# Optimization experiments

Measured on AMD Instinct MI355X. Metric: run time of the kernel, lower is better.

## Reference

```python
import jax, jax.numpy as jnp
import numpy as np

N_QUBITS = 20
W_MUL = (2.0 ** 0.5) * (5.0 ** -0.5)  # he_std = gain * 5**-0.5, use_wscale=True, lrmul=1

_C = jnp.complex64
X = jnp.array([[0, 1], [1, 0]], dtype=_C)
Y = jnp.array([[0, -1j], [1j, 0]], dtype=_C)
Z = jnp.array([[1, 0], [0, -1]], dtype=_C)
I2 = jnp.eye(2, dtype=_C)
I4 = jnp.eye(4, dtype=_C)
XX = jnp.kron(X, X)
YY = jnp.kron(Y, Y)
ZZ = jnp.kron(Z, Z)


def _rot(theta, pauli, ident):
    # exp(-i * theta/2 * P) = cos(theta/2) I - i sin(theta/2) P
    a = theta * 0.5
    return jnp.cos(a) * ident - (1j * jnp.sin(a)) * pauli


def _apply_1q(state, g, w):
    # state: [batch] + [2]*n ; contract gate input index with qubit axis w
    s = jnp.tensordot(g, state, axes=((1,), (w + 1,)))
    return jnp.moveaxis(s, 0, w + 1)


def _apply_2q(state, g4, w0, w1):
    g = g4.reshape(2, 2, 2, 2)  # (out0, out1, in0, in1)
    s = jnp.tensordot(g, state, axes=((2, 3), (w0 + 1, w1 + 1)))
    return jnp.moveaxis(s, (0, 1), (w0 + 1, w1 + 1))


def _xyz_layer(psi, params, n):
    # params: [3n]; rx, ry, rz on each wire
    for q in range(n):
        psi = _apply_1q(psi, _rot(params[3 * q], X, I2), q)
        psi = _apply_1q(psi, _rot(params[3 * q + 1], Y, I2), q)
        psi = _apply_1q(psi, _rot(params[3 * q + 2], Z, I2), q)
    return psi


def _circuit(psi, w, n):
    psi = _xyz_layer(psi, w[: 3 * n], n)
    for q in range(n - 1):
        i = 3 * n + 3 * q
        psi = _apply_2q(psi, _rot(w[i], XX, I4), q, q + 1)
        psi = _apply_2q(psi, _rot(w[i + 1], YY, I4), q, q + 1)
        psi = _apply_2q(psi, _rot(w[i + 2], ZZ, I4), q, q + 1)
    psi = _xyz_layer(psi, w[6 * n - 3 :], n)
    return psi


def setup_inputs() -> dict:
    key = jax.random.key(0)
    k1, k2 = jax.random.split(key)
    n = N_QUBITS
    dim = 1 << n
    batch = 4
    x = jax.random.normal(k1, (batch, 1, dim), dtype=jnp.float32)
    weight = jax.random.uniform(k2, (9 * n - 3,), dtype=jnp.float32, minval=0.0, maxval=2.0 * np.pi)
    return {"x": x, "weight": weight, "dimA": 10}


def reference(x, weight, dimA):
    n = N_QUBITS
    batch = x.shape[0]
    w = weight * W_MUL
    psi = x.astype(_C).reshape((batch,) + (2,) * n)  # MPS tensor [b, 2, ..., 2]
    psi = _circuit(psi, w, n)
    dimB = n - dimA
    # partial trace of |psi><psi| over the first dimB qubits (most-significant axes):
    # reduced[a, c] = sum_t psi[t, a] * conj(psi[t, c])  -- never materialize the full DM
    psi = psi.reshape(batch, 1 << dimB, 1 << dimA)
    rdm = jnp.einsum('bta,btc->bac', psi, psi.conj())
    # return real/imag stacked on last axis (real-valued representation of complex DM)
    return jnp.stack([rdm.real, rdm.imag], axis=-1)
```

## Files before the change

kernel.cpp:

```cpp
#include <hip/hip_runtime.h>
#include <hip/hip_bf16.h>

#define N_Q    20
#define DIM    (1 << N_Q)
#define BATCH  4
#define NGATES 19
#define L2OFF  117

typedef float2 c32;
typedef __attribute__((ext_vector_type(8))) short short8;
typedef __attribute__((ext_vector_type(4))) float f32x4;
typedef __attribute__((ext_vector_type(4))) unsigned int u32x4;

__device__ __forceinline__ c32 cmul(c32 a, c32 b) {
    return make_float2(fmaf(a.x, b.x, -a.y * b.y), fmaf(a.x, b.y, a.y * b.x));
}
__device__ __forceinline__ c32 cmadd(c32 acc, c32 a, c32 b) {
    acc.x = fmaf(a.x, b.x, fmaf(-a.y, b.y, acc.x));
    acc.y = fmaf(a.x, b.y, fmaf(a.y, b.x, acc.y));
    return acc;
}
__device__ __forceinline__ unsigned short f2bf(float f) {
    union { float f; unsigned u; } v; v.f = f;
    unsigned r = v.u + 0x7FFFu + ((v.u >> 16) & 1u);
    return (unsigned short)(r >> 16);
}
__device__ __forceinline__ void gll16(const void* g, void* l) {
    __builtin_amdgcn_global_load_lds((const __attribute__((address_space(1))) void*)g,
                                     (__attribute__((address_space(3))) void*)l, 16, 0, 0);
}

__device__ void mm2(const c32 A[2][2], const c32 B[2][2], c32 C[2][2]) {
    for (int i = 0; i < 2; i++)
        for (int j = 0; j < 2; j++) {
            c32 s = make_float2(0.f, 0.f);
            for (int k = 0; k < 2; k++) s = cmadd(s, A[i][k], B[k][j]);
            C[i][j] = s;
        }
}
__device__ void mm4(const c32 A[4][4], const c32 B[4][4], c32 C[4][4]) {
    for (int i = 0; i < 4; i++)
        for (int j = 0; j < 4; j++) {
            c32 s = make_float2(0.f, 0.f);
            for (int k = 0; k < 4; k++) s = cmadd(s, A[i][k], B[k][j]);
            C[i][j] = s;
        }
}
__device__ void single_u(const float* w, int base, c32 U[2][2]) {
    const float WM = 0.63245553203367586640f;
    float hx = w[base] * WM * 0.5f, hy = w[base + 1] * WM * 0.5f, hz = w[base + 2] * WM * 0.5f;
    float cx = cosf(hx), sx = sinf(hx);
    float cy = cosf(hy), sy = sinf(hy);
    float cz = cosf(hz), sz = sinf(hz);
    c32 RX[2][2] = {{{cx, 0.f}, {0.f, -sx}}, {{0.f, -sx}, {cx, 0.f}}};
    c32 RY[2][2] = {{{cy, 0.f}, {-sy, 0.f}}, {{sy, 0.f}, {cy, 0.f}}};
    c32 RZ[2][2] = {{{cz, -sz}, {0.f, 0.f}}, {{0.f, 0.f}, {cz, sz}}};
    c32 T[2][2];
    mm2(RY, RX, T);
    mm2(RZ, T, U);
}
__device__ void kron22(const c32 A[2][2], const c32 B[2][2], c32 K[4][4]) {
    for (int i = 0; i < 2; i++)
        for (int j = 0; j < 2; j++)
            for (int k = 0; k < 2; k++)
                for (int l = 0; l < 2; l++)
                    K[i * 2 + j][k * 2 + l] = cmul(A[i][k], B[j][l]);
}

__global__ void build_gates(const float* __restrict__ w, c32* __restrict__ G) {
    int q = threadIdx.x;
    if (q >= NGATES) return;
    const float WM = 0.63245553203367586640f;
    float hx = w[60 + 3 * q] * WM * 0.5f;
    float hy = w[61 + 3 * q] * WM * 0.5f;
    float hz = w[62 + 3 * q] * WM * 0.5f;
    float cx = cosf(hx), sx = sinf(hx);
    float cy = cosf(hy), sy = sinf(hy);
    float cz = cosf(hz), sz = sinf(hz);
    c32 RXX[4][4], RYY[4][4], RZZ[4][4];
    for (int i = 0; i < 4; i++)
        for (int j = 0; j < 4; j++) {
            RXX[i][j] = make_float2(0.f, 0.f);
            RYY[i][j] = make_float2(0.f, 0.f);
            RZZ[i][j] = make_float2(0.f, 0.f);
        }
    for (int i = 0; i < 4; i++) {
        RXX[i][i]     = make_float2(cx, 0.f);
        RXX[i][3 - i] = make_float2(0.f, -sx);
        RYY[i][i]     = make_float2(cy, 0.f);
    }
    RYY[0][3] = make_float2(0.f,  sy);
    RYY[1][2] = make_float2(0.f, -sy);
    RYY[2][1] = make_float2(0.f, -sy);
    RYY[3][0] = make_float2(0.f,  sy);
    RZZ[0][0] = make_float2(cz, -sz);
    RZZ[1][1] = make_float2(cz,  sz);
    RZZ[2][2] = make_float2(cz,  sz);
    RZZ[3][3] = make_float2(cz, -sz);
    c32 T[4][4], M[4][4];
    mm4(RYY, RXX, T);
    mm4(RZZ, T, M);

    c32 I2m[2][2] = {{{1.f, 0.f}, {0.f, 0.f}}, {{0.f, 0.f}, {1.f, 0.f}}};
    c32 Ua[2][2], Ub[2][2], Pre[4][4], Post[4][4];
    if (q == 0) {
        single_u(w, 0, Ua);
        single_u(w, 3, Ub);
        kron22(Ua, Ub, Pre);
    } else {
        single_u(w, 3 * (q + 1), Ub);
        kron22(I2m, Ub, Pre);
    }
    if (q == NGATES - 1) {
        single_u(w, L2OFF + 3 * 18, Ua);
        single_u(w, L2OFF + 3 * 19, Ub);
        kron22(Ua, Ub, Post);
    } else {
        single_u(w, L2OFF + 3 * q, Ua);
        kron22(Ua, I2m, Post);
    }
    c32 T2[4][4], Gq[4][4];
    mm4(M, Pre, T2);
    mm4(Post, T2, Gq);
    for (int i = 0; i < 4; i++)
        for (int j = 0; j < 4; j++)
            G[q * 16 + i * 4 + j] = Gq[i][j];
}

__device__ __forceinline__ void apply4(const c32* g, c32& x0, c32& x1, c32& x2, c32& x3) {
    c32 r0 = cmul(g[0],  x0); r0 = cmadd(r0, g[1],  x1); r0 = cmadd(r0, g[2],  x2); r0 = cmadd(r0, g[3],  x3);
    c32 r1 = cmul(g[4],  x0); r1 = cmadd(r1, g[5],  x1); r1 = cmadd(r1, g[6],  x2); r1 = cmadd(r1, g[7],  x3);
    c32 r2 = cmul(g[8],  x0); r2 = cmadd(r2, g[9],  x1); r2 = cmadd(r2, g[10], x2); r2 = cmadd(r2, g[11], x3);
    c32 r3 = cmul(g[12], x0); r3 = cmadd(r3, g[13], x1); r3 = cmadd(r3, g[14], x2); r3 = cmadd(r3, g[15], x3);
    x0 = r0; x1 = r1; x2 = r2; x3 = r3;
}
__device__ __forceinline__ void load_gate(const c32* __restrict__ gp, c32 g[16]) {
#pragma unroll
    for (int k = 0; k < 16; k++) g[k] = gp[k];
}
template <int LO>
__device__ __forceinline__ void gate_on32(c32 v[32], const c32 g[16]) {
#pragma unroll
    for (int m = 0; m < 8; ++m) {
        const int j0 = ((m >> LO) << (LO + 2)) | (m & ((1 << LO) - 1));
        const int s = 1 << LO;
        apply4(g, v[j0], v[j0 + s], v[j0 + 2 * s], v[j0 + 3 * s]);
    }
}
template <int LO>
__device__ __forceinline__ void gate_on16(c32* v, const c32 g[16]) {
#pragma unroll
    for (int m = 0; m < 4; ++m) {
        const int j0 = ((m >> LO) << (LO + 2)) | (m & ((1 << LO) - 1));
        const int s = 1 << LO;
        apply4(g, v[j0], v[j0 + s], v[j0 + 2 * s], v[j0 + 3 * s]);
    }
}

#define SIDX(l) ((l) ^ ((((l) >> 5) & 15)))

__global__ __launch_bounds__(256) void pass_a2(const float* __restrict__ x,
                                               c32* __restrict__ psi,
                                               const c32* __restrict__ Gall) {
    __shared__ __align__(16) char smem[65536];
    float* xs = (float*)smem;
    c32* s = (c32*)smem;
    int b = blockIdx.x >> 7;
    int c0 = (blockIdx.x & 127) << 5;
    const float* xp = x + ((size_t)b << 20) + c0;
    c32* pp = psi + ((size_t)b << 20) + c0;
    int t = threadIdx.x;
#pragma unroll
    for (int i = 0; i < 8; ++i) {
        int f4 = t + (i << 8);
        int row = f4 >> 3, sl = f4 & 7;
        float4 v = *reinterpret_cast<const float4*>(xp + (size_t)row * 4096 + sl * 4);
        reinterpret_cast<float4*>(xs)[row * 8 + (sl ^ (row & 7))] = v;
    }
    __syncthreads();
    int col = t & 31, rlow = t >> 5;
    c32 v[32], g[16];
#pragma unroll
    for (int j = 0; j < 32; ++j) {
        int row = (j << 3) | rlow;
        float re = xs[row * 32 + ((((col >> 2) ^ (row & 7)) << 2) | (col & 3))];
        v[j] = make_float2(re, 0.f);
    }
    __syncthreads();
    load_gate(Gall + 0 * 16, g);  gate_on32<3>(v, g);
    load_gate(Gall + 1 * 16, g);  gate_on32<2>(v, g);
    load_gate(Gall + 2 * 16, g);  gate_on32<1>(v, g);
    load_gate(Gall + 3 * 16, g);  gate_on32<0>(v, g);
#pragma unroll
    for (int j = 0; j < 32; ++j) {
        int l = ((((j << 3) | rlow) << 5)) | col;
        s[SIDX(l)] = v[j];
    }
    __syncthreads();
    int rhi = t >> 5;
#pragma unroll
    for (int rtop = 0; rtop < 2; ++rtop)
#pragma unroll
        for (int j = 0; j < 16; ++j) {
            int row = (rtop << 7) | (rhi << 4) | j;
            int l = (row << 5) | col;
            v[rtop * 16 + j] = s[SIDX(l)];
        }
    load_gate(Gall + 4 * 16, g);  gate_on16<2>(v, g);  gate_on16<2>(v + 16, g);
    load_gate(Gall + 5 * 16, g);  gate_on16<1>(v, g);  gate_on16<1>(v + 16, g);
    load_gate(Gall + 6 * 16, g);  gate_on16<0>(v, g);  gate_on16<0>(v + 16, g);
#pragma unroll
    for (int rtop = 0; rtop < 2; ++rtop)
#pragma unroll
        for (int j = 0; j < 16; ++j) {
            int row = (rtop << 7) | (rhi << 4) | j;
            pp[(size_t)row * 4096 + col] = v[rtop * 16 + j];
        }
}

__global__ __launch_bounds__(256) void pass_b2(const c32* __restrict__ psi,
                                               unsigned short* __restrict__ Brt,
                                               unsigned short* __restrict__ Bit,
                                               const c32* __restrict__ Gall) {
    __shared__ c32 s[8192];
    int b = blockIdx.x >> 7;
    int chunk = blockIdx.x & 127;
    const c32* pp = psi + ((size_t)b << 20) + ((size_t)chunk << 13);
    int t = threadIdx.x;
    c32 v[32], g[16];
#pragma unroll
    for (int j = 0; j < 32; ++j) v[j] = pp[(j << 8) | t];
    load_gate(Gall + 7 * 16, g);   gate_on32<3>(v, g);
    load_gate(Gall + 8 * 16, g);   gate_on32<2>(v, g);
    load_gate(Gall + 9 * 16, g);   gate_on32<1>(v, g);
    load_gate(Gall + 10 * 16, g);  gate_on32<0>(v, g);
#pragma unroll
    for (int j = 0; j < 32; ++j) { int l = (j << 8) | t; s[SIDX(l)] = v[j]; }
    __syncthreads();
    int hi2 = (t >> 4) << 9, lo2 = t & 15;
#pragma unroll
    for (int j = 0; j < 32; ++j) { int l = hi2 | (j << 4) | lo2; v[j] = s[SIDX(l)]; }
    load_gate(Gall + 11 * 16, g);  gate_on32<3>(v, g);
    load_gate(Gall + 12 * 16, g);  gate_on32<2>(v, g);
    load_gate(Gall + 13 * 16, g);  gate_on32<1>(v, g);
    load_gate(Gall + 14 * 16, g);  gate_on32<0>(v, g);
    __syncthreads();
#pragma unroll
    for (int j = 0; j < 32; ++j) { int l = hi2 | (j << 4) | lo2; s[SIDX(l)] = v[j]; }
    __syncthreads();
#pragma unroll
    for (int j = 0; j < 32; ++j) { int l = (t << 5) | j; v[j] = s[SIDX(l)]; }
    load_gate(Gall + 15 * 16, g);  gate_on32<3>(v, g);
    load_gate(Gall + 16 * 16, g);  gate_on32<2>(v, g);
    load_gate(Gall + 17 * 16, g);  gate_on32<1>(v, g);
    load_gate(Gall + 18 * 16, g);  gate_on32<0>(v, g);
    size_t off = ((size_t)b << 20) + ((size_t)chunk << 13) + ((size_t)t << 5);
#pragma unroll
    for (int p = 0; p < 4; ++p) {
        unsigned short rr[8], ri[8];
#pragma unroll
        for (int i = 0; i < 8; ++i) {
            rr[i] = f2bf(v[8 * p + i].x);
            ri[i] = f2bf(v[8 * p + i].y);
        }
        *reinterpret_cast<float4*>(Brt + off + 8 * p) = *reinterpret_cast<float4*>(rr);
        *reinterpret_cast<float4*>(Bit + off + 8 * p) = *reinterpret_cast<float4*>(ri);
    }
}

__global__ __launch_bounds__(256) void bt_t(const unsigned short* __restrict__ Brt,
                                            const unsigned short* __restrict__ Bit,
                                            unsigned short* __restrict__ Art,
                                            unsigned short* __restrict__ Ait) {
    __shared__ unsigned lds32[64 * 66];
    int b  = blockIdx.z;
    int t0 = blockIdx.x * 64;
    int a0 = blockIdx.y * 64;
    size_t gb = (size_t)b << 20;
#pragma unroll
    for (int h = 0; h < 2; ++h) {
        int p = threadIdx.x + h * 256;
        int r = p >> 3, cq = p & 7;
        size_t src = gb + (size_t)(t0 + r) * 1024 + a0 + cq * 8;
        float4 fr = *reinterpret_cast<const float4*>(Brt + src);
        float4 fi = *reinterpret_cast<const float4*>(Bit + src);
        const unsigned short* ur = reinterpret_cast<const unsigned short*>(&fr);
        const unsigned short* ui = reinterpret_cast<const unsigned short*>(&fi);
#pragma unroll
        for (int i = 0; i < 8; ++i)
            lds32[r * 66 + cq * 8 + i] = (unsigned)ur[i] | ((unsigned)ui[i] << 16);
    }
    __syncthreads();
#pragma unroll
    for (int h = 0; h < 2; ++h) {
        int q = threadIdx.x + h * 256;
        int a = q >> 3, tq = q & 7;
        unsigned short rr[8], ri[8];
#pragma unroll
        for (int i = 0; i < 8; ++i) {
            unsigned w = lds32[(tq * 8 + i) * 66 + a];
            rr[i] = (unsigned short)(w & 0xFFFF);
            ri[i] = (unsigned short)(w >> 16);
        }
        size_t dst = gb + (size_t)(a0 + a) * 1024 + t0 + tq * 8;
        *reinterpret_cast<float4*>(Art + dst) = *reinterpret_cast<float4*>(rr);
        *reinterpret_cast<float4*>(Ait + dst) = *reinterpret_cast<float4*>(ri);
    }
}

__device__ __forceinline__ void stage_panel(const unsigned short* __restrict__ sp, size_t gb,
                                            int prow, int kt, unsigned short* dst, int lane) {
    int srow = lane >> 3, sslot = lane & 7;
#pragma unroll
    for (int i = 0; i < 8; ++i) {
        int r = (i << 3) | srow;
        int sl = sslot ^ srow;
        const unsigned short* gp = sp + gb + ((size_t)(prow + r) << 10) + kt * 64 + sl * 8;
        gll16(gp, dst + i * 512);
    }
}
__global__ __launch_bounds__(256) void gram_mfma2(const unsigned short* __restrict__ Art,
                                                  const unsigned short* __restrict__ Ait,
                                                  float2* __restrict__ out) {
    __shared__ unsigned short lds[2][4][4096];
    int b = blockIdx.y;
    int rem = blockIdx.x;
    int ia = 0;
    while (rem >= 16 - ia) { rem -= 16 - ia; ++ia; }
    int ic = ia + rem;
    int a0 = ia * 64, c0 = ic * 64;
    int lane = threadIdx.x & 63, w = threadIdx.x >> 6;
    int wr = (w >> 1) * 32, wc = (w & 1) * 32;
    const unsigned short* sp = (w & 1) ? Ait : Art;
    int prow = (w < 2) ? a0 : c0;
    size_t gb = (size_t)b << 20;

    f32x4 accRe[2][2], accIm[2][2];
#pragma unroll
    for (int m = 0; m < 2; m++)
#pragma unroll
        for (int n = 0; n < 2; n++) { accRe[m][n] = (f32x4)0.f; accIm[m][n] = (f32x4)0.f; }

    stage_panel(sp, gb, prow, 0, &lds[0][w][0], lane);
    __syncthreads();
    for (int kt = 0; kt < 16; ++kt) {
        int cur = kt & 1;
        if (kt < 15) stage_panel(sp, gb, prow, kt + 1, &lds[cur ^ 1][w][0], lane);
#pragma unroll
        for (int kk = 0; kk < 2; ++kk) {
            int sbase = kk * 4 + (lane >> 4);
            short8 ar[2], ai[2], br[2], bi[2];
#pragma unroll
            for (int m = 0; m < 2; m++) {
                int r = wr + m * 16 + (lane & 15);
                int off = r * 64 + ((sbase ^ (r & 7)) << 3);
                ar[m] = *reinterpret_cast<const short8*>(&lds[cur][0][off]);
                ai[m] = *reinterpret_cast<const short8*>(&lds[cur][1][off]);
            }
#pragma unroll
            for (int n = 0; n < 2; n++) {
                int r = wc + n * 16 + (lane & 15);
                int off = r * 64 + ((sbase ^ (r & 7)) << 3);
                br[n] = *reinterpret_cast<const short8*>(&lds[cur][2][off]);
                bi[n] = *reinterpret_cast<const short8*>(&lds[cur][3][off]);
            }
#pragma unroll
            for (int m = 0; m < 2; m++) {
                u32x4 tn = *reinterpret_cast<u32x4*>(&ar[m]) ^ 0x80008000u;
                short8 arn = *reinterpret_cast<short8*>(&tn);
#pragma unroll
                for (int n = 0; n < 2; n++) {
                    accRe[m][n] = __builtin_amdgcn_mfma_f32_16x16x32_bf16(ar[m],  br[n], accRe[m][n], 0, 0, 0);
                    accRe[m][n] = __builtin_amdgcn_mfma_f32_16x16x32_bf16(ai[m],  bi[n], accRe[m][n], 0, 0, 0);
                    accIm[m][n] = __builtin_amdgcn_mfma_f32_16x16x32_bf16(ai[m],  br[n], accIm[m][n], 0, 0, 0);
                    accIm[m][n] = __builtin_amdgcn_mfma_f32_16x16x32_bf16(arn,    bi[n], accIm[m][n], 0, 0, 0);
                }
            }
        }
        __syncthreads();
    }
    size_t ob = (size_t)b << 20;
#pragma unroll
    for (int m = 0; m < 2; m++)
#pragma unroll
        for (int n = 0; n < 2; n++)
#pragma unroll
            for (int r = 0; r < 4; r++) {
                int a = a0 + wr + m * 16 + (lane >> 4) * 4 + r;
                int c = c0 + wc + n * 16 + (lane & 15);
                float re = accRe[m][n][r];
                float im = accIm[m][n][r];
                out[ob + ((size_t)a << 10) + c] = make_float2(re, im);
                if (ia != ic)
                    out[ob + ((size_t)c << 10) + a] = make_float2(re, -im);
            }
}

extern "C" void kernel_launch(void* const* d_in, const int* in_sizes, int n_in,
                              void* d_out, int out_size, void* d_ws, size_t ws_size,
                              hipStream_t stream) {
    const float* x = (const float*)d_in[0];
    const float* weight = (const float*)d_in[1];
    const size_t psiBytes = (size_t)BATCH * DIM * sizeof(c32);
    c32* psi = (c32*)d_ws;
    c32* G = (c32*)((char*)d_ws + psiBytes);
    unsigned short* Brt = (unsigned short*)((char*)d_ws + psiBytes + 65536);
    unsigned short* Bit = Brt + (size_t)BATCH * DIM;
    unsigned short* Art = Bit + (size_t)BATCH * DIM;
    unsigned short* Ait = Art + (size_t)BATCH * DIM;

    build_gates<<<1, 64, 0, stream>>>(weight, G);
    pass_a2<<<BATCH * 128, 256, 0, stream>>>(x, psi, G);
    pass_b2<<<BATCH * 128, 256, 0, stream>>>(psi, Brt, Bit, G);
    bt_t<<<dim3(16, 16, BATCH), 256, 0, stream>>>(Brt, Bit, Art, Ait);
    gram_mfma2<<<dim3(136, BATCH), 256, 0, stream>>>(Art, Ait, (float2*)d_out);
}
```

Baseline: 106.7 us.

## Split gram kernel K-tiles across 8 waves with LDS reduction and XCD-aware block remap

The Gram MFMA kernel now runs 512 threads per block. Each pair of waves splits the two 32-wide k-subtiles of every 64-wide K tile, and the partial accumulators are reduced through LDS at the end. The double-buffered staging is replaced by a single buffer, with loads issued in the same iteration followed by a barrier. Block indices are also remapped across the eight XCDs so neighbouring tiles share L2. The goal is more waves per CU to hide latency and better cache locality, at the cost of losing the prefetch overlap and adding a reduction step.

```diff
diff --git a/kernel.cpp b/kernel.cpp
--- a/kernel.cpp
+++ b/kernel.cpp
@@ -308,31 +308,26 @@
     }
 }
 
-__device__ __forceinline__ void stage_panel(const unsigned short* __restrict__ sp, size_t gb,
-                                            int prow, int kt, unsigned short* dst, int lane) {
-    int srow = lane >> 3, sslot = lane & 7;
-#pragma unroll
-    for (int i = 0; i < 8; ++i) {
-        int r = (i << 3) | srow;
-        int sl = sslot ^ srow;
-        const unsigned short* gp = sp + gb + ((size_t)(prow + r) << 10) + kt * 64 + sl * 8;
-        gll16(gp, dst + i * 512);
-    }
-}
-__global__ __launch_bounds__(256) void gram_mfma2(const unsigned short* __restrict__ Art,
+__global__ __launch_bounds__(512) void gram_mfma4(const unsigned short* __restrict__ Art,
                                                   const unsigned short* __restrict__ Ait,
                                                   float2* __restrict__ out) {
-    __shared__ unsigned short lds[2][4][4096];
-    int b = blockIdx.y;
-    int rem = blockIdx.x;
+    __shared__ __align__(16) unsigned short lds[4][4096];
+    int hw = blockIdx.y * 136 + blockIdx.x;
+    int virt = (hw & 7) * 68 + (hw >> 3);
+    int b = virt / 136;
+    int rem = virt - b * 136;
     int ia = 0;
     while (rem >= 16 - ia) { rem -= 16 - ia; ++ia; }
     int ic = ia + rem;
     int a0 = ia * 64, c0 = ic * 64;
-    int lane = threadIdx.x & 63, w = threadIdx.x >> 6;
-    int wr = (w >> 1) * 32, wc = (w & 1) * 32;
-    const unsigned short* sp = (w & 1) ? Ait : Art;
-    int prow = (w < 2) ? a0 : c0;
+    int tid = threadIdx.x;
+    int lane = tid & 63, w = tid >> 6;
+    int q = w & 3, kk0 = w >> 2;
+    int wr = (q >> 1) * 32, wc = (q & 1) * 32;
+    int arr = w >> 1, half = w & 1;
+    const unsigned short* sp = (arr & 1) ? Ait : Art;
+    int prow = (arr < 2) ? a0 : c0;
+    int srow = lane >> 3, sslot = lane & 7;
     size_t gb = (size_t)b << 20;
 
     f32x4 accRe[2][2], accIm[2][2];
@@ -341,28 +336,31 @@
 #pragma unroll
         for (int n = 0; n < 2; n++) { accRe[m][n] = (f32x4)0.f; accIm[m][n] = (f32x4)0.f; }
 
-    stage_panel(sp, gb, prow, 0, &lds[0][w][0], lane);
-    __syncthreads();
     for (int kt = 0; kt < 16; ++kt) {
-        int cur = kt & 1;
-        if (kt < 15) stage_panel(sp, gb, prow, kt + 1, &lds[cur ^ 1][w][0], lane);
-#pragma unroll
-        for (int kk = 0; kk < 2; ++kk) {
-            int sbase = kk * 4 + (lane >> 4);
+#pragma unroll
+        for (int i = 0; i < 4; ++i) {
+            int r = (half << 5) | (i << 3) | srow;
+            int sl = sslot ^ srow;
+            const unsigned short* gp = sp + gb + ((size_t)(prow + r) << 10) + kt * 64 + sl * 8;
+            gll16(gp, &lds[arr][(half << 11) + (i << 9) + lane * 8]);
+        }
+        __syncthreads();
+        {
+            int sbase = kk0 * 4 + (lane >> 4);
             short8 ar[2], ai[2], br[2], bi[2];
 #pragma unroll
             for (int m = 0; m < 2; m++) {
                 int r = wr + m * 16 + (lane & 15);
                 int off = r * 64 + ((sbase ^ (r & 7)) << 3);
-                ar[m] = *reinterpret_cast<const short8*>(&lds[cur][0][off]);
-                ai[m] = *reinterpret_cast<const short8*>(&lds[cur][1][off]);
+                ar[m] = *reinterpret_cast<const short8*>(&lds[0][off]);
+                ai[m] = *reinterpret_cast<const short8*>(&lds[1][off]);
             }
 #pragma unroll
             for (int n = 0; n < 2; n++) {
                 int r = wc + n * 16 + (lane & 15);
                 int off = r * 64 + ((sbase ^ (r & 7)) << 3);
-                br[n] = *reinterpret_cast<const short8*>(&lds[cur][2][off]);
-                bi[n] = *reinterpret_cast<const short8*>(&lds[cur][3][off]);
+                br[n] = *reinterpret_cast<const short8*>(&lds[2][off]);
+                bi[n] = *reinterpret_cast<const short8*>(&lds[3][off]);
             }
 #pragma unroll
             for (int m = 0; m < 2; m++) {
@@ -379,21 +377,47 @@
         }
         __syncthreads();
     }
-    size_t ob = (size_t)b << 20;
-#pragma unroll
-    for (int m = 0; m < 2; m++)
-#pragma unroll
-        for (int n = 0; n < 2; n++)
-#pragma unroll
-            for (int r = 0; r < 4; r++) {
-                int a = a0 + wr + m * 16 + (lane >> 4) * 4 + r;
-                int c = c0 + wc + n * 16 + (lane & 15);
-                float re = accRe[m][n][r];
-                float im = accIm[m][n][r];
-                out[ob + ((size_t)a << 10) + c] = make_float2(re, im);
-                if (ia != ic)
-                    out[ob + ((size_t)c << 10) + a] = make_float2(re, -im);
-            }
+    float* xch = reinterpret_cast<float*>(&lds[0][0]);
+    if (kk0 == 1) {
+        float* dst = xch + q * 2048 + lane * 4;
+        int idx = 0;
+#pragma unroll
+        for (int m = 0; m < 2; m++)
+#pragma unroll
+            for (int n = 0; n < 2; n++) { *reinterpret_cast<f32x4*>(dst + idx * 256) = accRe[m][n]; idx++; }
+#pragma unroll
+        for (int m = 0; m < 2; m++)
+#pragma unroll
+            for (int n = 0; n < 2; n++) { *reinterpret_cast<f32x4*>(dst + idx * 256) = accIm[m][n]; idx++; }
+    }
+    __syncthreads();
+    if (kk0 == 0) {
+        float* src = xch + q * 2048 + lane * 4;
+        int idx = 0;
+#pragma unroll
+        for (int m = 0; m < 2; m++)
+#pragma unroll
+            for (int n = 0; n < 2; n++) { accRe[m][n] += *reinterpret_cast<f32x4*>(src + idx * 256); idx++; }
+#pragma unroll
+        for (int m = 0; m < 2; m++)
+#pragma unroll
+            for (int n = 0; n < 2; n++) { accIm[m][n] += *reinterpret_cast<f32x4*>(src + idx * 256); idx++; }
+        size_t ob = (size_t)b << 20;
+#pragma unroll
+        for (int m = 0; m < 2; m++)
+#pragma unroll
+            for (int n = 0; n < 2; n++)
+#pragma unroll
+                for (int r = 0; r < 4; r++) {
+                    int a = a0 + wr + m * 16 + (lane >> 4) * 4 + r;
+                    int c = c0 + wc + n * 16 + (lane & 15);
+                    float re = accRe[m][n][r];
+                    float im = accIm[m][n][r];
+                    out[ob + ((size_t)a << 10) + c] = make_float2(re, im);
+                    if (ia != ic)
+                        out[ob + ((size_t)c << 10) + a] = make_float2(re, -im);
+                }
+    }
 }
 
 extern "C" void kernel_launch(void* const* d_in, const int* in_sizes, int n_in,
@@ -413,5 +437,5 @@
     pass_a2<<<BATCH * 128, 256, 0, stream>>>(x, psi, G);
     pass_b2<<<BATCH * 128, 256, 0, stream>>>(psi, Brt, Bit, G);
     bt_t<<<dim3(16, 16, BATCH), 256, 0, stream>>>(Brt, Bit, Art, Ait);
-    gram_mfma2<<<dim3(136, BATCH), 256, 0, stream>>>(Art, Ait, (float2*)d_out);
-}
+    gram_mfma4<<<dim3(136, BATCH), 512, 0, stream>>>(Art, Ait, (float2*)d_out);
+}
```

Result: no change. 107.8 us (+1.1%).
